# Performance work log

Measured on AMD Instinct MI355X. Metric: run time of the kernel, lower is better.

Reference implementation:

```python
import jax, jax.numpy as jnp
import numpy as np

NHEAD = 16
EPS = 1e-5


def layer_norm(x, w, b):
    mu = jnp.mean(x, axis=-1, keepdims=True)
    var = jnp.var(x, axis=-1, keepdims=True)
    return (x - mu) * jax.lax.rsqrt(var + EPS) * w + b


def setup_inputs() -> dict:
    key = jax.random.key(0)
    ks = jax.random.split(key, 14)
    B, S, E, F = 16, 1024, 1024, 4096
    s = 0.02
    return {
        "x": jax.random.normal(ks[0], (B, S, E), jnp.float32),
        "in_proj_w": jax.random.normal(ks[1], (3 * E, E), jnp.float32) * s,
        "in_proj_b": jax.random.normal(ks[2], (3 * E,), jnp.float32) * s,
        "out_w": jax.random.normal(ks[3], (E, E), jnp.float32) * s,
        "out_b": jax.random.normal(ks[4], (E,), jnp.float32) * s,
        "lin1_w": jax.random.normal(ks[5], (F, E), jnp.float32) * s,
        "lin1_b": jax.random.normal(ks[6], (F,), jnp.float32) * s,
        "lin2_w": jax.random.normal(ks[7], (E, F), jnp.float32) * s,
        "lin2_b": jax.random.normal(ks[8], (E,), jnp.float32) * s,
        "norm1_w": jnp.ones((E,), jnp.float32),
        "norm1_b": jnp.zeros((E,), jnp.float32),
        "norm2_w": jnp.ones((E,), jnp.float32),
        "norm2_b": jnp.zeros((E,), jnp.float32),
    }


def reference(x, in_proj_w, in_proj_b, out_w, out_b, lin1_w, lin1_b, lin2_w, lin2_b,
              norm1_w, norm1_b, norm2_w, norm2_b):
    B, S, E = x.shape
    H = NHEAD
    D = E // H

    # --- pre-norm self-attention (q = k = v = norm1(x)) ---
    xn = layer_norm(x, norm1_w, norm1_b)
    qkv = xn @ in_proj_w.T + in_proj_b                      # [B,S,3E]
    q, k, v = jnp.split(qkv, 3, axis=-1)
    q = q.reshape(B, S, H, D)
    k = k.reshape(B, S, H, D)
    v = v.reshape(B, S, H, D)
    scale = 1.0 / jnp.sqrt(jnp.asarray(D, x.dtype))
    scores = jnp.einsum("bqhd,bkhd->bhqk", q, k) * scale    # [B,H,S,S]
    attn = jax.nn.softmax(scores, axis=-1)
    ctx = jnp.einsum("bhqk,bkhd->bqhd", attn, v).reshape(B, S, E)
    attn_out = ctx @ out_w.T + out_b
    x = x + attn_out

    # --- pre-norm feedforward (gelu) ---
    xn2 = layer_norm(x, norm2_w, norm2_b)
    h = jax.nn.gelu(xn2 @ lin1_w.T + lin1_b, approximate=False)
    x = x + (h @ lin2_w.T + lin2_b)
    return x
```

## Files before the change

kernel.cpp:

```cpp
#include <hip/hip_runtime.h>


typedef __attribute__((ext_vector_type(8))) short bf16x8;
typedef __attribute__((ext_vector_type(4))) float f32x4;
typedef __attribute__((ext_vector_type(8))) unsigned short u16x8;
typedef __attribute__((ext_vector_type(4))) unsigned short u16x4;

__device__ __forceinline__ float bf2f(unsigned short u) {
    return __uint_as_float(((unsigned int)u) << 16);
}
__device__ __forceinline__ unsigned short f2bf(float f) {
    unsigned int u = __float_as_uint(f);
    u += 0x7fffu + ((u >> 16) & 1u);
    return (unsigned short)(u >> 16);
}
__device__ __forceinline__ unsigned int pkbf_trunc(float a, float b) {
    return (__float_as_uint(a) >> 16) | (__float_as_uint(b) & 0xffff0000u);
}

__device__ __forceinline__ void gload_lds16(const unsigned short* g, unsigned short* l) {
    __builtin_amdgcn_global_load_lds(
        (const __attribute__((address_space(1))) unsigned int*)g,
        (__attribute__((address_space(3))) unsigned int*)l, 16, 0, 0);
}

__global__ __launch_bounds__(256) void cvt_kernel(const float* __restrict__ in,
                                                  unsigned short* __restrict__ out, int n4) {
    int i = blockIdx.x * 256 + threadIdx.x;
    if (i >= n4) return;
    float4 v = ((const float4*)in)[i];
    u16x4 o;
    o[0] = f2bf(v.x); o[1] = f2bf(v.y); o[2] = f2bf(v.z); o[3] = f2bf(v.w);
    ((u16x4*)out)[i] = o;
}

__global__ __launch_bounds__(256) void ln_kernel(const float* __restrict__ x,
                                                 const float* __restrict__ w,
                                                 const float* __restrict__ b,
                                                 unsigned short* __restrict__ out) {
    const int row = blockIdx.x;
    const int t = threadIdx.x;
    const float* xr = x + (size_t)row * 1024;
    float4 v = *(const float4*)(xr + t * 4);
    float s = v.x + v.y + v.z + v.w;
    float sq = v.x * v.x + v.y * v.y + v.z * v.z + v.w * v.w;
#pragma unroll
    for (int off = 32; off > 0; off >>= 1) {
        s += __shfl_xor(s, off);
        sq += __shfl_xor(sq, off);
    }
    __shared__ float rs_[4], rq_[4];
    if ((t & 63) == 0) { rs_[t >> 6] = s; rq_[t >> 6] = sq; }
    __syncthreads();
    s = rs_[0] + rs_[1] + rs_[2] + rs_[3];
    sq = rq_[0] + rq_[1] + rq_[2] + rq_[3];
    const float mu = s * (1.0f / 1024.0f);
    const float var = sq * (1.0f / 1024.0f) - mu * mu;
    const float rstd = rsqrtf(var + 1e-5f);
    const int c = t * 4;
    float4 wv = *(const float4*)(w + c);
    float4 bv = *(const float4*)(b + c);
    u16x4 o;
    o[0] = f2bf((v.x - mu) * rstd * wv.x + bv.x);
    o[1] = f2bf((v.y - mu) * rstd * wv.y + bv.y);
    o[2] = f2bf((v.z - mu) * rstd * wv.z + bv.z);
    o[3] = f2bf((v.w - mu) * rstd * wv.w + bv.w);
    *(u16x4*)(out + (size_t)row * 1024 + c) = o;
}

template <int EPI>
__global__ __launch_bounds__(256) void gemm_bt(const unsigned short* __restrict__ A,
                                               const unsigned short* __restrict__ Bt,
                                               const float* __restrict__ bias,
                                               const float* __restrict__ resid,
                                               void* __restrict__ outp,
                                               int M, int N, int K) {
    __shared__ __align__(16) unsigned short sA[128 * 64];
    __shared__ __align__(16) unsigned short sB[128 * 64];
    const int t = threadIdx.x;
    const int lane = t & 63;
    const int w = t >> 6;
    const int wm = (w >> 1) * 64;
    const int wn = (w & 1) * 64;
    const int quad = lane >> 4;
    const int cl = lane & 15;
    const int mBase = blockIdx.y * 128;
    const int nBase = blockIdx.x * 128;

    const int rg = lane >> 3;
    const int gc = (lane & 7) ^ rg;
    const unsigned short* gA = A + (size_t)(mBase + w * 32 + rg) * K + gc * 8;
    const unsigned short* gB = Bt + (size_t)(nBase + w * 32 + rg) * K + gc * 8;

    f32x4 acc[4][4] = {};

    for (int k0 = 0; k0 < K; k0 += 64) {
#pragma unroll
        for (int u = 0; u < 4; ++u) {
            gload_lds16(gA + (size_t)u * 8 * K + k0, sA + (w * 4 + u) * 512);
            gload_lds16(gB + (size_t)u * 8 * K + k0, sB + (w * 4 + u) * 512);
        }
        __syncthreads();
#pragma unroll
        for (int ks = 0; ks < 2; ++ks) {
            bf16x8 af[4], bfr[4];
#pragma unroll
            for (int i = 0; i < 4; ++i) {
                const int ra = wm + i * 16 + cl;
                af[i] = *(const bf16x8*)(sA + ra * 64 + (((quad + 4 * ks) ^ (ra & 7)) * 8));
                const int rb = wn + i * 16 + cl;
                bfr[i] = *(const bf16x8*)(sB + rb * 64 + (((quad + 4 * ks) ^ (rb & 7)) * 8));
            }
#pragma unroll
            for (int i = 0; i < 4; ++i)
#pragma unroll
                for (int j = 0; j < 4; ++j)
                    acc[i][j] = __builtin_amdgcn_mfma_f32_16x16x32_bf16(af[i], bfr[j],
                                                                        acc[i][j], 0, 0, 0);
        }
        __syncthreads();
    }

#pragma unroll
    for (int i = 0; i < 4; ++i) {
        const int rowg = mBase + wm + i * 16 + quad * 4;
#pragma unroll
        for (int j = 0; j < 4; ++j) {
            const int colg = nBase + wn + j * 16 + cl;
            const float bv = bias[colg];
#pragma unroll
            for (int rr = 0; rr < 4; ++rr) {
                const float v = acc[i][j][rr] + bv;
                const size_t idx = (size_t)(rowg + rr) * N + colg;
                if constexpr (EPI == 0) {
                    ((unsigned short*)outp)[idx] = f2bf(v);
                } else if constexpr (EPI == 1) {
                    ((float*)outp)[idx] = v + resid[idx];
                } else {
                    const float g = 0.5f * v * (1.0f + erff(v * 0.70710678118654752f));
                    ((unsigned short*)outp)[idx] = f2bf(g);
                }
            }
        }
    }
}

__global__ __launch_bounds__(256) void attn_mfma(const unsigned short* __restrict__ qkv,
                                                 unsigned short* __restrict__ ctx) {
    __shared__ __align__(16) unsigned short Ks[64 * 72];
    __shared__ __align__(16) unsigned int Vt[64 * 36];
    __shared__ __align__(16) unsigned short Ps[128 * 72];

    const int bh = blockIdx.x;
    const int qt = blockIdx.y;
    const int b = bh >> 4;
    const int h = bh & 15;
    const int t = threadIdx.x;
    const int w = t >> 6;
    const int lane = t & 63;
    const int quad = lane >> 4;
    const int cl = lane & 15;
    const size_t tok0 = (size_t)b * 1024;
    const int qrow0 = qt * 128 + w * 32;

    bf16x8 aq[2][2];
#pragma unroll
    for (int sub = 0; sub < 2; ++sub) {
        const unsigned short* qp =
            qkv + (tok0 + qrow0 + sub * 16 + cl) * 3072 + h * 64 + quad * 8;
        aq[sub][0] = *(const bf16x8*)(qp);
        aq[sub][1] = *(const bf16x8*)(qp + 32);
    }

    const bf16x8 vones = {0x3F80, 0x3F80, 0x3F80, 0x3F80, 0x3F80, 0x3F80, 0x3F80, 0x3F80};

    const int r0 = t >> 2;
    const int c16 = (t & 3) * 16;
    const int kp = t >> 3;
    const int dc = t & 7;

    f32x4 acc[2][5] = {};
    float m_r[2] = {-3.0e38f, -3.0e38f};

    for (int kt = 0; kt < 16; ++kt) {
        {
            const unsigned short* kg =
                qkv + (tok0 + kt * 64 + r0) * 3072 + 1024 + h * 64 + c16;
            *(int4*)(Ks + r0 * 72 + c16) = *(const int4*)(kg);
            *(int4*)(Ks + r0 * 72 + c16 + 8) = *(const int4*)(kg + 8);

            const unsigned short* vg =
                qkv + (tok0 + kt * 64 + 2 * kp) * 3072 + 2048 + h * 64 + dc * 8;
            u16x8 v0 = *(const u16x8*)(vg);
            u16x8 v1 = *(const u16x8*)(vg + 3072);
            const int g = kp >> 2, wd = kp & 3;
#pragma unroll
            for (int j = 0; j < 8; ++j) {
                const int d = dc * 8 + j;
                Vt[d * 36 + (((g ^ (d >> 3)) << 2) | wd)] =
                    ((unsigned int)v1[j] << 16) | (unsigned int)v0[j];
            }
        }
        __syncthreads();

#pragma unroll
        for (int sub = 0; sub < 2; ++sub) {
            f32x4 sc[4] = {};
#pragma unroll
            for (int i = 0; i < 4; ++i) {
                const int rb = i * 16 + cl;
#pragma unroll
                for (int ks = 0; ks < 2; ++ks) {
                    bf16x8 bk = *(const bf16x8*)(Ks + rb * 72 + quad * 8 + ks * 32);
                    sc[i] = __builtin_amdgcn_mfma_f32_16x16x32_bf16(bk, aq[sub][ks], sc[i],
                                                                    0, 0, 0);
                }
            }
            float mx0 = fmaxf(fmaxf(sc[0][0], sc[0][1]), fmaxf(sc[0][2], sc[0][3]));
            float mx1 = fmaxf(fmaxf(sc[1][0], sc[1][1]), fmaxf(sc[1][2], sc[1][3]));
            float mx2 = fmaxf(fmaxf(sc[2][0], sc[2][1]), fmaxf(sc[2][2], sc[2][3]));
            float mx3 = fmaxf(fmaxf(sc[3][0], sc[3][1]), fmaxf(sc[3][2], sc[3][3]));
            float rmax = fmaxf(fmaxf(mx0, mx1), fmaxf(mx2, mx3));
            rmax = fmaxf(rmax, __shfl_xor(rmax, 16));
            rmax = fmaxf(rmax, __shfl_xor(rmax, 32));
            const float mnew = fmaxf(m_r[sub], rmax * 0.125f);
            const float alpha = __expf(m_r[sub] - mnew);
            m_r[sub] = mnew;
            float al[4];
#pragma unroll
            for (int rr = 0; rr < 4; ++rr) al[rr] = __shfl(alpha, quad * 4 + rr, 16);
#pragma unroll
            for (int j = 0; j < 5; ++j)
#pragma unroll
                for (int rr = 0; rr < 4; ++rr) acc[sub][j][rr] *= al[rr];
            const unsigned short* pr = Ps + (w * 32 + sub * 16 + cl) * 72;
#pragma unroll
            for (int i = 0; i < 4; ++i) {
                const float p0 = __expf(fmaf(sc[i][0], 0.125f, -mnew));
                const float p1 = __expf(fmaf(sc[i][1], 0.125f, -mnew));
                const float p2 = __expf(fmaf(sc[i][2], 0.125f, -mnew));
                const float p3 = __expf(fmaf(sc[i][3], 0.125f, -mnew));
                uint2 pk;
                pk.x = pkbf_trunc(p0, p1);
                pk.y = pkbf_trunc(p2, p3);
                *(uint2*)(pr + i * 16 + quad * 4) = pk;
            }
        }

#pragma unroll
        for (int ks = 0; ks < 2; ++ks) {
            bf16x8 bv[4];
#pragma unroll
            for (int j = 0; j < 4; ++j) {
                const int d = j * 16 + cl;
                bv[j] = *(const bf16x8*)(Vt + d * 36 + (((quad + 4 * ks) ^ (d >> 3)) << 2));
            }
#pragma unroll
            for (int sub = 0; sub < 2; ++sub) {
                bf16x8 ap =
                    *(const bf16x8*)(Ps + (w * 32 + sub * 16 + cl) * 72 + quad * 8 + ks * 32);
#pragma unroll
                for (int j = 0; j < 4; ++j)
                    acc[sub][j] =
                        __builtin_amdgcn_mfma_f32_16x16x32_bf16(ap, bv[j], acc[sub][j], 0, 0, 0);
                acc[sub][4] =
                    __builtin_amdgcn_mfma_f32_16x16x32_bf16(ap, vones, acc[sub][4], 0, 0, 0);
            }
        }
        __syncthreads();
    }

#pragma unroll
    for (int sub = 0; sub < 2; ++sub)
#pragma unroll
        for (int rr = 0; rr < 4; ++rr) {
            const float inv = 1.0f / acc[sub][4][rr];
            const size_t tok = tok0 + qt * 128 + w * 32 + sub * 16 + quad * 4 + rr;
#pragma unroll
            for (int j = 0; j < 4; ++j)
                ctx[tok * 1024 + h * 64 + j * 16 + cl] = f2bf(acc[sub][j][rr] * inv);
        }
}

extern "C" void kernel_launch(void* const* d_in, const int* in_sizes, int n_in,
                              void* d_out, int out_size, void* d_ws, size_t ws_size,
                              hipStream_t stream) {
    const float* x    = (const float*)d_in[0];
    const float* wqkv = (const float*)d_in[1];
    const float* bqkv = (const float*)d_in[2];
    const float* wo   = (const float*)d_in[3];
    const float* bo   = (const float*)d_in[4];
    const float* w1   = (const float*)d_in[5];
    const float* b1   = (const float*)d_in[6];
    const float* w2   = (const float*)d_in[7];
    const float* b2   = (const float*)d_in[8];
    const float* n1w  = (const float*)d_in[9];
    const float* n1b  = (const float*)d_in[10];
    const float* n2w  = (const float*)d_in[11];
    const float* n2b  = (const float*)d_in[12];
    float* out = (float*)d_out;

    char* ws = (char*)d_ws;
    unsigned short* wqkv_b = (unsigned short*)(ws);
    unsigned short* wo_b   = (unsigned short*)(ws + 6291456);
    unsigned short* w1_b   = (unsigned short*)(ws + 8388608);
    unsigned short* w2_b   = (unsigned short*)(ws + 16777216);
    unsigned short* r1     = (unsigned short*)(ws + 25165824);
    unsigned short* r2     = (unsigned short*)(ws + 58720256);

    unsigned short* xn_b  = r1;
    unsigned short* ctx_b = r1;
    unsigned short* xn2_b = r1;
    unsigned short* qkv_b = r2;
    unsigned short* h_b   = r2;

    cvt_kernel<<<3072, 256, 0, stream>>>(wqkv, wqkv_b, 786432);
    cvt_kernel<<<1024, 256, 0, stream>>>(wo, wo_b, 262144);
    cvt_kernel<<<4096, 256, 0, stream>>>(w1, w1_b, 1048576);
    cvt_kernel<<<4096, 256, 0, stream>>>(w2, w2_b, 1048576);

    ln_kernel<<<16384, 256, 0, stream>>>(x, n1w, n1b, xn_b);
    gemm_bt<0><<<dim3(24, 128), 256, 0, stream>>>(xn_b, wqkv_b, bqkv, nullptr, qkv_b,
                                                  16384, 3072, 1024);
    attn_mfma<<<dim3(256, 8), 256, 0, stream>>>(qkv_b, ctx_b);
    gemm_bt<1><<<dim3(8, 128), 256, 0, stream>>>(ctx_b, wo_b, bo, x, out, 16384, 1024, 1024);
    ln_kernel<<<16384, 256, 0, stream>>>(out, n2w, n2b, xn2_b);

    if (ws_size >= 192937984ULL) {
        gemm_bt<2><<<dim3(32, 128), 256, 0, stream>>>(xn2_b, w1_b, b1, nullptr, h_b,
                                                      16384, 4096, 1024);
        gemm_bt<1><<<dim3(8, 128), 256, 0, stream>>>(h_b, w2_b, b2, out, out,
                                                     16384, 1024, 4096);
    } else {
        for (int c = 0; c < 2; ++c) {
            const size_t row0 = (size_t)c * 8192;
            gemm_bt<2><<<dim3(32, 64), 256, 0, stream>>>(xn2_b + row0 * 1024, w1_b, b1,
                                                         nullptr, h_b, 8192, 4096, 1024);
            gemm_bt<1><<<dim3(8, 64), 256, 0, stream>>>(h_b, w2_b, b2, out + row0 * 1024,
                                                        out + row0 * 1024, 8192, 1024, 4096);
        }
    }
}
```

Before: 913.9 us.

## Rewrite GEMM as 256x256 tiles with double-buffered LDS pipeline and 8 waves

The bf16 GEMM moves from 128x128 tiles with 4 waves and a single LDS buffer to 256x256 tiles with 8 waves, double-buffered LDS, and explicit vmcnt waits. Global-to-LDS loads for the next K slice are interleaved with MFMA quarters under barriers and setprio. The workgroup index is remapped so that consecutive blocks are spread across XCDs. The aim is to hide load latency, raise arithmetic intensity and improve L2 reuse, at the cost of 128KB of LDS per block, higher register pressure, and fewer blocks in flight for the smaller GEMMs.

```diff
diff --git a/kernel.cpp b/kernel.cpp
--- a/kernel.cpp
+++ b/kernel.cpp
@@ -23,6 +23,19 @@
         (const __attribute__((address_space(1))) unsigned int*)g,
         (__attribute__((address_space(3))) unsigned int*)l, 16, 0, 0);
 }
+
+#define FENCE() asm volatile("" ::: "memory")
+#define BAR()                         \
+    do {                              \
+        FENCE();                      \
+        __builtin_amdgcn_s_barrier(); \
+        FENCE();                      \
+    } while (0)
+#define VMCNT(n)                                               \
+    do {                                                       \
+        asm volatile("s_waitcnt vmcnt(" #n ")" ::: "memory");  \
+        __builtin_amdgcn_sched_barrier(0);                     \
+    } while (0)
 
 __global__ __launch_bounds__(256) void cvt_kernel(const float* __restrict__ in,
                                                   unsigned short* __restrict__ out, int n4) {
@@ -69,68 +82,131 @@
 }
 
 template <int EPI>
-__global__ __launch_bounds__(256) void gemm_bt(const unsigned short* __restrict__ A,
-                                               const unsigned short* __restrict__ Bt,
-                                               const float* __restrict__ bias,
-                                               const float* __restrict__ resid,
-                                               void* __restrict__ outp,
-                                               int M, int N, int K) {
-    __shared__ __align__(16) unsigned short sA[128 * 64];
-    __shared__ __align__(16) unsigned short sB[128 * 64];
+__global__ __launch_bounds__(512, 2) void gemm_bt(const unsigned short* __restrict__ A,
+                                                  const unsigned short* __restrict__ Bt,
+                                                  const float* __restrict__ bias,
+                                                  const float* __restrict__ resid,
+                                                  void* __restrict__ outp,
+                                                  int M, int N, int K) {
+    __shared__ __align__(16) unsigned short sA[2][256 * 64];
+    __shared__ __align__(16) unsigned short sB[2][256 * 64];
     const int t = threadIdx.x;
     const int lane = t & 63;
     const int w = t >> 6;
-    const int wm = (w >> 1) * 64;
-    const int wn = (w & 1) * 64;
+    const int wm = w >> 2;
+    const int wn = w & 3;
     const int quad = lane >> 4;
     const int cl = lane & 15;
-    const int mBase = blockIdx.y * 128;
-    const int nBase = blockIdx.x * 128;
-
-    const int rg = lane >> 3;
-    const int gc = (lane & 7) ^ rg;
-    const unsigned short* gA = A + (size_t)(mBase + w * 32 + rg) * K + gc * 8;
-    const unsigned short* gB = Bt + (size_t)(nBase + w * 32 + rg) * K + gc * 8;
-
-    f32x4 acc[4][4] = {};
-
-    for (int k0 = 0; k0 < K; k0 += 64) {
-#pragma unroll
-        for (int u = 0; u < 4; ++u) {
-            gload_lds16(gA + (size_t)u * 8 * K + k0, sA + (w * 4 + u) * 512);
-            gload_lds16(gB + (size_t)u * 8 * K + k0, sB + (w * 4 + u) * 512);
-        }
-        __syncthreads();
-#pragma unroll
-        for (int ks = 0; ks < 2; ++ks) {
-            bf16x8 af[4], bfr[4];
-#pragma unroll
-            for (int i = 0; i < 4; ++i) {
-                const int ra = wm + i * 16 + cl;
-                af[i] = *(const bf16x8*)(sA + ra * 64 + (((quad + 4 * ks) ^ (ra & 7)) * 8));
-                const int rb = wn + i * 16 + cl;
-                bfr[i] = *(const bf16x8*)(sB + rb * 64 + (((quad + 4 * ks) ^ (rb & 7)) * 8));
-            }
-#pragma unroll
-            for (int i = 0; i < 4; ++i)
-#pragma unroll
-                for (int j = 0; j < 4; ++j)
-                    acc[i][j] = __builtin_amdgcn_mfma_f32_16x16x32_bf16(af[i], bfr[j],
-                                                                        acc[i][j], 0, 0, 0);
-        }
-        __syncthreads();
-    }
-
-#pragma unroll
-    for (int i = 0; i < 4; ++i) {
-        const int rowg = mBase + wm + i * 16 + quad * 4;
-#pragma unroll
-        for (int j = 0; j < 4; ++j) {
-            const int colg = nBase + wn + j * 16 + cl;
+
+    const int nwg = gridDim.x * gridDim.y;
+    int wg = blockIdx.y * gridDim.x + blockIdx.x;
+    wg = (wg & 7) * (nwg >> 3) + (wg >> 3);
+    const int mBase = (wg / gridDim.x) * 256;
+    const int nBase = (wg % gridDim.x) * 256;
+
+    const int rl = lane >> 3;
+    const int ch = ((lane & 7) ^ rl) * 8;
+    const unsigned short* gA = A + (size_t)mBase * K;
+    const unsigned short* gB = Bt + (size_t)nBase * K;
+
+#define STAGE_A(buf, hf, k0)                                                          \
+    do {                                                                              \
+        _Pragma("unroll") for (int u_ = 0; u_ < 2; ++u_) {                            \
+            const int r_ = (hf) * 128 + (w * 2 + u_) * 8;                             \
+            gload_lds16(gA + (size_t)(r_ + rl) * K + (k0) + ch, &sA[buf][r_ * 64]);   \
+        }                                                                             \
+    } while (0)
+#define STAGE_B(buf, hf, k0)                                                          \
+    do {                                                                              \
+        _Pragma("unroll") for (int u_ = 0; u_ < 2; ++u_) {                            \
+            const int r_ = (hf) * 128 + (w * 2 + u_) * 8;                             \
+            gload_lds16(gB + (size_t)(r_ + rl) * K + (k0) + ch, &sB[buf][r_ * 64]);   \
+        }                                                                             \
+    } while (0)
+#define READ_B8(buf)                                                                  \
+    do {                                                                              \
+        _Pragma("unroll") for (int nf_ = 0; nf_ < 4; ++nf_) {                         \
+            const int rb_ = wn * 64 + nf_ * 16 + cl;                                  \
+            _Pragma("unroll") for (int ks_ = 0; ks_ < 2; ++ks_)                       \
+                bf[nf_][ks_] = *(const bf16x8*)(&sB[buf][rb_ * 64 +                   \
+                                     (((quad + 4 * ks_) ^ (rb_ & 7)) * 8)]);          \
+        }                                                                             \
+    } while (0)
+#define READ_A2(buf, mfb)                                                             \
+    do {                                                                              \
+        _Pragma("unroll") for (int m_ = 0; m_ < 2; ++m_) {                            \
+            const int ra_ = wm * 128 + ((mfb) + m_) * 16 + cl;                        \
+            _Pragma("unroll") for (int ks_ = 0; ks_ < 2; ++ks_)                       \
+                af[m_][ks_] = *(const bf16x8*)(&sA[buf][ra_ * 64 +                    \
+                                     (((quad + 4 * ks_) ^ (ra_ & 7)) * 8)]);          \
+        }                                                                             \
+    } while (0)
+#define MFMA_Q(q)                                                                     \
+    do {                                                                              \
+        __builtin_amdgcn_s_setprio(1);                                                \
+        _Pragma("unroll") for (int m_ = 0; m_ < 2; ++m_)                              \
+            _Pragma("unroll") for (int nf_ = 0; nf_ < 4; ++nf_)                       \
+                _Pragma("unroll") for (int ks_ = 0; ks_ < 2; ++ks_)                   \
+                    acc[2 * (q) + m_][nf_] = __builtin_amdgcn_mfma_f32_16x16x32_bf16( \
+                        af[m_][ks_], bf[nf_][ks_], acc[2 * (q) + m_][nf_], 0, 0, 0);  \
+        __builtin_amdgcn_s_setprio(0);                                                \
+    } while (0)
+
+    f32x4 acc[8][4] = {};
+    bf16x8 bf[4][2];
+    bf16x8 af[2][2];
+
+    STAGE_A(0, 0, 0); STAGE_A(0, 1, 0);
+    STAGE_B(0, 0, 0); STAGE_B(0, 1, 0);
+    STAGE_B(1, 0, 64); STAGE_B(1, 1, 64);
+    VMCNT(4);
+    BAR();
+
+    const int NI = K >> 7;
+    for (int i = 0; i < NI; ++i) {
+        const bool more = (i + 1 < NI);
+        const int kT1 = (i << 7) + 64;
+        const int kN = (i + 1) << 7;
+        READ_B8(0); READ_A2(0, 0);
+        STAGE_A(1, 0, kT1);
+        BAR(); MFMA_Q(0); BAR();
+        READ_A2(0, 2);
+        STAGE_A(1, 1, kT1);
+        BAR(); MFMA_Q(1); BAR();
+        READ_A2(0, 4);
+        if (more) STAGE_B(0, 0, kN);
+        BAR(); MFMA_Q(2); BAR();
+        READ_A2(0, 6);
+        if (more) STAGE_B(0, 1, kN);
+        BAR(); MFMA_Q(3);
+        if (more) { VMCNT(4); } else { VMCNT(0); }
+        BAR();
+        READ_B8(1); READ_A2(1, 0);
+        if (more) STAGE_A(0, 0, kN);
+        BAR(); MFMA_Q(0); BAR();
+        READ_A2(1, 2);
+        if (more) STAGE_A(0, 1, kN);
+        BAR(); MFMA_Q(1); BAR();
+        READ_A2(1, 4);
+        if (more) STAGE_B(1, 0, kN + 64);
+        BAR(); MFMA_Q(2); BAR();
+        READ_A2(1, 6);
+        if (more) STAGE_B(1, 1, kN + 64);
+        BAR(); MFMA_Q(3);
+        if (more) VMCNT(4);
+        BAR();
+    }
+
+#pragma unroll
+    for (int mf = 0; mf < 8; ++mf) {
+        const int rowg = mBase + wm * 128 + mf * 16 + quad * 4;
+#pragma unroll
+        for (int nf = 0; nf < 4; ++nf) {
+            const int colg = nBase + wn * 64 + nf * 16 + cl;
             const float bv = bias[colg];
 #pragma unroll
             for (int rr = 0; rr < 4; ++rr) {
-                const float v = acc[i][j][rr] + bv;
+                const float v = acc[mf][nf][rr] + bv;
                 const size_t idx = (size_t)(rowg + rr) * N + colg;
                 if constexpr (EPI == 0) {
                     ((unsigned short*)outp)[idx] = f2bf(v);
@@ -143,6 +219,11 @@
             }
         }
     }
+#undef STAGE_A
+#undef STAGE_B
+#undef READ_B8
+#undef READ_A2
+#undef MFMA_Q
 }
 
 __global__ __launch_bounds__(256) void attn_mfma(const unsigned short* __restrict__ qkv,
@@ -320,23 +401,23 @@
     cvt_kernel<<<4096, 256, 0, stream>>>(w2, w2_b, 1048576);
 
     ln_kernel<<<16384, 256, 0, stream>>>(x, n1w, n1b, xn_b);
-    gemm_bt<0><<<dim3(24, 128), 256, 0, stream>>>(xn_b, wqkv_b, bqkv, nullptr, qkv_b,
-                                                  16384, 3072, 1024);
+    gemm_bt<0><<<dim3(12, 64), 512, 0, stream>>>(xn_b, wqkv_b, bqkv, nullptr, qkv_b,
+                                                 16384, 3072, 1024);
     attn_mfma<<<dim3(256, 8), 256, 0, stream>>>(qkv_b, ctx_b);
-    gemm_bt<1><<<dim3(8, 128), 256, 0, stream>>>(ctx_b, wo_b, bo, x, out, 16384, 1024, 1024);
+    gemm_bt<1><<<dim3(4, 64), 512, 0, stream>>>(ctx_b, wo_b, bo, x, out, 16384, 1024, 1024);
     ln_kernel<<<16384, 256, 0, stream>>>(out, n2w, n2b, xn2_b);
 
     if (ws_size >= 192937984ULL) {
-        gemm_bt<2><<<dim3(32, 128), 256, 0, stream>>>(xn2_b, w1_b, b1, nullptr, h_b,
-                                                      16384, 4096, 1024);
-        gemm_bt<1><<<dim3(8, 128), 256, 0, stream>>>(h_b, w2_b, b2, out, out,
-                                                     16384, 1024, 4096);
+        gemm_bt<2><<<dim3(16, 64), 512, 0, stream>>>(xn2_b, w1_b, b1, nullptr, h_b,
+                                                     16384, 4096, 1024);
+        gemm_bt<1><<<dim3(4, 64), 512, 0, stream>>>(h_b, w2_b, b2, out, out,
+                                                    16384, 1024, 4096);
     } else {
         for (int c = 0; c < 2; ++c) {
             const size_t row0 = (size_t)c * 8192;
-            gemm_bt<2><<<dim3(32, 64), 256, 0, stream>>>(xn2_b + row0 * 1024, w1_b, b1,
+            gemm_bt<2><<<dim3(16, 32), 512, 0, stream>>>(xn2_b + row0 * 1024, w1_b, b1,
                                                          nullptr, h_b, 8192, 4096, 1024);
-            gemm_bt<1><<<dim3(8, 64), 256, 0, stream>>>(h_b, w2_b, b2, out + row0 * 1024,
+            gemm_bt<1><<<dim3(4, 32), 512, 0, stream>>>(h_b, w2_b, b2, out + row0 * 1024,
                                                         out + row0 * 1024, 8192, 1024, 4096);
         }
     }
```

After: 873.4 us. -4.4%, faster.
